# Optimization experiments

Measured on AMD Instinct MI355X. Metric: run time of the kernel, lower is better.

Reference implementation:

```python
import jax, jax.numpy as jnp
import numpy as np

B, T, C = 2, 2048, 1024
E = 1024          # total attention embedding (head_size arg of TransformerBlock)
H = 16            # n_heads
HS = E // H       # per-head size = 64
FF = 4 * C        # ffwd_mul * in_embd
EPS = 1e-5


def setup_inputs() -> dict:
    key = jax.random.key(0)
    ks = jax.random.split(key, 20)
    s = lambda fan_in: 1.0 / np.sqrt(fan_in)
    return {
        "x":     jax.random.normal(ks[0], (B, T, C), jnp.float32),
        "Wq":    jax.random.normal(ks[1], (C, E), jnp.float32) * s(C),
        "bq":    jnp.zeros((E,), jnp.float32),
        "Wk":    jax.random.normal(ks[2], (C, E), jnp.float32) * s(C),
        "bk":    jnp.zeros((E,), jnp.float32),
        "Wv":    jax.random.normal(ks[3], (C, E), jnp.float32) * s(C),
        "bv":    jnp.zeros((E,), jnp.float32),
        "Wo":    jax.random.normal(ks[4], (E, C), jnp.float32) * s(E),
        "bo":    jnp.zeros((C,), jnp.float32),
        "ln1_g": jnp.ones((C,), jnp.float32),
        "ln1_b": jnp.zeros((C,), jnp.float32),
        "W1":    jax.random.normal(ks[5], (C, FF), jnp.float32) * s(C),
        "b1":    jnp.zeros((FF,), jnp.float32),
        "W2":    jax.random.normal(ks[6], (FF, C), jnp.float32) * s(FF),
        "b2":    jnp.zeros((C,), jnp.float32),
        "ln2_g": jnp.ones((C,), jnp.float32),
        "ln2_b": jnp.zeros((C,), jnp.float32),
        "Wc":    jax.random.normal(ks[7], (C, C), jnp.float32) * s(C),
        "bc":    jnp.zeros((C,), jnp.float32),
    }


def _layernorm(x, g, b):
    mu = jnp.mean(x, axis=-1, keepdims=True)
    var = jnp.mean(jnp.square(x - mu), axis=-1, keepdims=True)
    return (x - mu) * jax.lax.rsqrt(var + EPS) * g + b


def _attention(x, Wq, bq, Wk, bk, Wv, bv, Wo, bo):
    # batched equivalent of the per-head Linear q/k/v loop + concat
    q = (x @ Wq + bq).reshape(B, T, H, HS)
    k = (x @ Wk + bk).reshape(B, T, H, HS)
    v = (x @ Wv + bv).reshape(B, T, H, HS)
    scores = jnp.einsum("bthd,bshd->bhts", q, k) / np.sqrt(HS)  # no causal mask in source
    wei = jax.nn.softmax(scores, axis=-1)
    out = jnp.einsum("bhts,bshd->bthd", wei, v).reshape(B, T, E)
    return out @ Wo + bo


def reference(x, Wq, bq, Wk, bk, Wv, bv, Wo, bo, ln1_g, ln1_b,
              W1, b1, W2, b2, ln2_g, ln2_b, Wc, bc):
    out = _layernorm(x + _attention(x, Wq, bq, Wk, bk, Wv, bv, Wo, bo), ln1_g, ln1_b)
    ff = jax.nn.gelu(out @ W1 + b1, approximate=False) @ W2 + b2  # torch GELU is exact erf
    out = _layernorm(out + ff, ln2_g, ln2_b)
    # Conv1d(C, C, kernel_size=1) over transposed input == pointwise linear
    out = out @ Wc.T + bc
    return out
```

## Files before the change

### kernel.cpp

```cpp
#include <hip/hip_runtime.h>
#include <hip/hip_bf16.h>
#include <cstdint>
#include <cstddef>

#define DEVINL __device__ __forceinline__

typedef __attribute__((ext_vector_type(4)))  float f32x4;
typedef __attribute__((ext_vector_type(16))) float f32x16;
typedef __attribute__((ext_vector_type(8)))  short s16x8;

#define QSCALE 0.1803368801111204f

DEVINL short f2bf(float f) {
  union { float f; unsigned u; } v; v.f = f;
  unsigned r = (v.u + 0x7fffu + ((v.u >> 16) & 1u)) >> 16;
  return (short)r;
}

DEVINL void gload_lds16(const void* g, void* l) {
  __builtin_amdgcn_global_load_lds((const __attribute__((address_space(1))) void*)g,
                                   (__attribute__((address_space(3))) void*)l,
                                   16, 0, 0);
}

DEVINL s16x8 lds_frag(const short* base, int row, int cb) {
  const int addr = row * 128 + (cb ^ ((row & 7) << 4));
  return *(const s16x8*)((const char*)base + addr);
}

enum { EPI_F32 = 0, EPI_GELU = 1, EPI_RES = 2, EPI_QKV = 3 };

template <int EPI, int BM>
__global__ __launch_bounds__(256) void gemm_bt(
    const short* __restrict__ A, const short* __restrict__ Bt,
    const float* __restrict__ bias, const float* __restrict__ res,
    float* __restrict__ outF, short* __restrict__ outB,
    short* __restrict__ qp, short* __restrict__ kp, short* __restrict__ vt,
    int M, int N, int K)
{
  constexpr int MI = BM / 32;
  constexpr int CAW = BM / 64;
  __shared__ short As[BM * 32];
  __shared__ short Bs[128 * 32];
  const int tid = threadIdx.x;
  const int w = tid >> 6, lane = tid & 63;
  const int wr = w >> 1, wc = w & 1;

  const int gx = gridDim.x;
  int id = blockIdx.x + gx * blockIdx.y;
  const int cpx = (gx * gridDim.y) >> 3;
  id = (id & 7) * cpx + (id >> 3);
  const int n0 = (id % gx) * 128, m0 = (id / gx) * BM;

  const int lrow = lane >> 2, lk = (lane & 3) << 3;
  const short* Ag = A + (size_t)m0 * K;
  const short* Bg = Bt + (size_t)n0 * K;

  f32x4 acc[MI][4] = {};

  for (int kk = 0; kk < K; kk += 32) {
#pragma unroll
    for (int i = 0; i < CAW; ++i) {
      const int c = w * CAW + i;
      gload_lds16(Ag + (size_t)(c * 16 + lrow) * K + (kk + lk), &As[c * 512]);
    }
#pragma unroll
    for (int i = 0; i < 2; ++i) {
      const int c = w * 2 + i;
      gload_lds16(Bg + (size_t)(c * 16 + lrow) * K + (kk + lk), &Bs[c * 512]);
    }
    __syncthreads();
    s16x8 af[MI], bf[4];
#pragma unroll
    for (int mi = 0; mi < MI; ++mi)
      af[mi] = *(const s16x8*)&As[(wr * (BM / 2) + mi * 16 + (lane & 15)) * 32 + ((lane >> 4) << 3)];
#pragma unroll
    for (int ni = 0; ni < 4; ++ni)
      bf[ni] = *(const s16x8*)&Bs[(wc * 64 + ni * 16 + (lane & 15)) * 32 + ((lane >> 4) << 3)];
#pragma unroll
    for (int mi = 0; mi < MI; ++mi)
#pragma unroll
      for (int ni = 0; ni < 4; ++ni)
        acc[mi][ni] = __builtin_amdgcn_mfma_f32_16x16x32_bf16(af[mi], bf[ni], acc[mi][ni], 0, 0, 0);
    __syncthreads();
  }

  const int rbase = m0 + wr * (BM / 2) + ((lane >> 4) << 2);
  const int cbase = n0 + wc * 64 + (lane & 15);
#pragma unroll
  for (int mi = 0; mi < MI; ++mi) {
#pragma unroll
    for (int ni = 0; ni < 4; ++ni) {
      const int col = cbase + ni * 16;
      const float bv = bias[col];
      if (EPI == EPI_QKV) {
        const int e = col & 1023, id3 = col >> 10;
        const int h = e >> 6, d = e & 63;
        const int row0 = rbase + mi * 16;
        const int b = row0 >> 11, t0 = row0 & 2047;
        if (id3 == 0) {
#pragma unroll
          for (int j = 0; j < 4; ++j)
            qp[((size_t)(b * 16 + h) * 2048 + t0 + j) * 64 + d] = f2bf((acc[mi][ni][j] + bv) * QSCALE);
        } else if (id3 == 1) {
#pragma unroll
          for (int j = 0; j < 4; ++j)
            kp[((size_t)(b * 16 + h) * 2048 + t0 + j) * 64 + d] = f2bf(acc[mi][ni][j] + bv);
        } else {
          short4 pk4;
          pk4.x = f2bf(acc[mi][ni][0] + bv); pk4.y = f2bf(acc[mi][ni][1] + bv);
          pk4.z = f2bf(acc[mi][ni][2] + bv); pk4.w = f2bf(acc[mi][ni][3] + bv);
          *(short4*)&vt[((size_t)(b * 16 + h) * 64 + d) * 2048 + t0] = pk4;
        }
      } else {
#pragma unroll
        for (int j = 0; j < 4; ++j) {
          const int row = rbase + mi * 16 + j;
          float v = acc[mi][ni][j] + bv;
          if (EPI == EPI_GELU) {
            outB[(size_t)row * N + col] = f2bf(0.5f * v * (1.0f + erff(v * 0.70710678118654752f)));
          } else if (EPI == EPI_RES) {
            outF[(size_t)row * N + col] = v + res[(size_t)row * N + col];
          } else {
            outF[(size_t)row * N + col] = v;
          }
        }
      }
    }
  }
}

__global__ __launch_bounds__(256) void attn_kernel(
    const short* __restrict__ qg, const short* __restrict__ kg,
    const short* __restrict__ vtg, short* __restrict__ outB)
{
  __shared__ short Ks[2][64 * 64];
  __shared__ short Vs[2][64 * 64];
  __shared__ float sbuf[4][32];

  const int bh = blockIdx.x, qb = blockIdx.y;
  const int tid = threadIdx.x, w = tid >> 6, lane = tid & 63;
  const int b = bh >> 4, h = bh & 15;
  const int ql = lane & 31, hi = lane >> 5;
  const int qrow = qb * 128 + w * 32 + ql;

  s16x8 qf[4];
  const short* qrp = qg + ((size_t)bh * 2048 + qrow) * 64;
#pragma unroll
  for (int kd = 0; kd < 4; ++kd)
    qf[kd] = *(const s16x8*)(qrp + kd * 16 + hi * 8);

  f32x16 o[2] = {};
  float mrow = -3.0e38f, lsum = 0.f;

  const size_t kbase = (size_t)bh * 2048 * 64;
  const size_t vbase = (size_t)bh * 64 * 2048;

#define STAGE(t, bufi)                                                         \
  {                                                                            \
    _Pragma("unroll") for (int i = 0; i < 2; ++i) {                            \
      const int pb = i * 4096 + w * 1024;                                      \
      const int p = pb + lane * 16;                                            \
      const int row = p >> 7;                                                  \
      const int cs = (p & 127) ^ ((row & 7) << 4);                             \
      gload_lds16(kg + kbase + (size_t)((t) * 64 + row) * 64 + (cs >> 1),      \
                  &Ks[bufi][pb >> 1]);                                         \
      gload_lds16(vtg + vbase + (size_t)row * 2048 + (t) * 64 + (cs >> 1),     \
                  &Vs[bufi][pb >> 1]);                                         \
    }                                                                          \
  }

  STAGE(0, 0);
  __syncthreads();

  for (int t = 0; t < 32; ++t) {
    const int buf = t & 1;
    if (t < 31) STAGE(t + 1, buf ^ 1);
    const short* kb = Ks[buf];
    const short* vb = Vs[buf];

    f32x16 pS[2] = {};
#pragma unroll
    for (int kd = 0; kd < 4; ++kd) {
      const s16x8 a0 = lds_frag(kb, ql,      kd * 32 + hi * 16);
      const s16x8 a1 = lds_frag(kb, 32 + ql, kd * 32 + hi * 16);
      pS[0] = __builtin_amdgcn_mfma_f32_32x32x16_bf16(a0, qf[kd], pS[0], 0, 0, 0);
      pS[1] = __builtin_amdgcn_mfma_f32_32x32x16_bf16(a1, qf[kd], pS[1], 0, 0, 0);
    }

    float pm = pS[0][0];
#pragma unroll
    for (int r = 1; r < 16; ++r) pm = fmaxf(pm, pS[0][r]);
#pragma unroll
    for (int r = 0; r < 16; ++r) pm = fmaxf(pm, pS[1][r]);
    pm = fmaxf(pm, __shfl_xor(pm, 32));

    if (!__all(pm <= mrow + 8.0f)) {
      const float mnew = fmaxf(mrow, pm);
      const float alpha = exp2f(mrow - mnew);
      mrow = mnew;
      lsum *= alpha;
      sbuf[w][ql] = alpha;
#pragma unroll
      for (int r = 0; r < 16; ++r) {
        const float a = sbuf[w][(r & 3) + 8 * (r >> 2) + 4 * hi];
        o[0][r] *= a; o[1][r] *= a;
      }
    }

    float rs = 0.f;
#pragma unroll
    for (int r = 0; r < 16; ++r) { pS[0][r] = exp2f(pS[0][r] - mrow); rs += pS[0][r]; }
#pragma unroll
    for (int r = 0; r < 16; ++r) { pS[1][r] = exp2f(pS[1][r] - mrow); rs += pS[1][r]; }
    rs += __shfl_xor(rs, 32);
    lsum += rs;

#pragma unroll
    for (int ks = 0; ks < 4; ++ks) {
      const int tI = ks >> 1, b8 = (ks & 1) * 8;
      unsigned u0, u1, v0, v1;
      asm("v_cvt_pk_bf16_f32 %0, %1, %2" : "=v"(u0) : "v"(pS[tI][b8 + 0]), "v"(pS[tI][b8 + 1]));
      asm("v_cvt_pk_bf16_f32 %0, %1, %2" : "=v"(u1) : "v"(pS[tI][b8 + 2]), "v"(pS[tI][b8 + 3]));
      asm("v_cvt_pk_bf16_f32 %0, %1, %2" : "=v"(v0) : "v"(pS[tI][b8 + 4]), "v"(pS[tI][b8 + 5]));
      asm("v_cvt_pk_bf16_f32 %0, %1, %2" : "=v"(v1) : "v"(pS[tI][b8 + 6]), "v"(pS[tI][b8 + 7]));
      const unsigned su0 = (unsigned)__shfl_xor((int)u0, 32);
      const unsigned su1 = (unsigned)__shfl_xor((int)u1, 32);
      const unsigned sv0 = (unsigned)__shfl_xor((int)v0, 32);
      const unsigned sv1 = (unsigned)__shfl_xor((int)v1, 32);
      union { unsigned u[4]; s16x8 s; } pa;
      pa.u[0] = hi ? sv0 : u0;
      pa.u[1] = hi ? sv1 : u1;
      pa.u[2] = hi ? v0 : su0;
      pa.u[3] = hi ? v1 : su1;
      const s16x8 vf0 = lds_frag(vb, ql,      ks * 32 + hi * 16);
      const s16x8 vf1 = lds_frag(vb, 32 + ql, ks * 32 + hi * 16);
      o[0] = __builtin_amdgcn_mfma_f32_32x32x16_bf16(pa.s, vf0, o[0], 0, 0, 0);
      o[1] = __builtin_amdgcn_mfma_f32_32x32x16_bf16(pa.s, vf1, o[1], 0, 0, 0);
    }
    __syncthreads();
  }

  sbuf[w][ql] = lsum;
#pragma unroll
  for (int r = 0; r < 16; ++r) {
    const int q = (r & 3) + 8 * (r >> 2) + 4 * hi;
    const float linv = 1.0f / sbuf[w][q];
    const int tq = qb * 128 + w * 32 + q;
    const size_t orow = ((size_t)b * 2048 + tq) * 1024 + h * 64;
    outB[orow + ql]      = f2bf(o[0][r] * linv);
    outB[orow + 32 + ql] = f2bf(o[1][r] * linv);
  }
}

__global__ __launch_bounds__(256) void ln_kernel(
    const float* in, float* outF, short* __restrict__ outB,
    const float* __restrict__ gw, const float* __restrict__ bw)
{
  const int row = blockIdx.x, tid = threadIdx.x;
  const float4 v = ((const float4*)(in + (size_t)row * 1024))[tid];
  float s = v.x + v.y + v.z + v.w;
  float s2 = v.x * v.x + v.y * v.y + v.z * v.z + v.w * v.w;
#pragma unroll
  for (int m = 1; m < 64; m <<= 1) { s += __shfl_xor(s, m); s2 += __shfl_xor(s2, m); }
  __shared__ float as1[4], as2[4];
  if ((tid & 63) == 0) { as1[tid >> 6] = s; as2[tid >> 6] = s2; }
  __syncthreads();
  s = as1[0] + as1[1] + as1[2] + as1[3];
  s2 = as2[0] + as2[1] + as2[2] + as2[3];
  const float mu = s * (1.f / 1024.f);
  const float var = s2 * (1.f / 1024.f) - mu * mu;
  const float rstd = rsqrtf(var + 1e-5f);
  const float4 g = ((const float4*)gw)[tid];
  const float4 bb = ((const float4*)bw)[tid];
  float4 y;
  y.x = (v.x - mu) * rstd * g.x + bb.x;
  y.y = (v.y - mu) * rstd * g.y + bb.y;
  y.z = (v.z - mu) * rstd * g.z + bb.z;
  y.w = (v.w - mu) * rstd * g.w + bb.w;
  ((float4*)(outF + (size_t)row * 1024))[tid] = y;
  short4 ob; ob.x = f2bf(y.x); ob.y = f2bf(y.y); ob.z = f2bf(y.z); ob.w = f2bf(y.w);
  ((short4*)(outB + (size_t)row * 1024))[tid] = ob;
}

__global__ __launch_bounds__(256) void transpose_cast(
    const float* __restrict__ src, short* __restrict__ dst, int R, int Cc)
{
  __shared__ float tile[32][33];
  const int c0 = blockIdx.x * 32, r0 = blockIdx.y * 32;
  const int x = threadIdx.x & 31, y = threadIdx.x >> 5;
#pragma unroll
  for (int i = 0; i < 32; i += 8)
    tile[y + i][x] = src[(size_t)(r0 + y + i) * Cc + c0 + x];
  __syncthreads();
#pragma unroll
  for (int i = 0; i < 32; i += 8)
    dst[(size_t)(c0 + y + i) * R + r0 + x] = f2bf(tile[x][y + i]);
}

__global__ __launch_bounds__(256) void cast_bf16_kernel(
    const float* __restrict__ src, short* __restrict__ dst, int n4)
{
  const int i = blockIdx.x * 256 + threadIdx.x;
  if (i < n4) {
    const float4 v = ((const float4*)src)[i];
    short4 o; o.x = f2bf(v.x); o.y = f2bf(v.y); o.z = f2bf(v.z); o.w = f2bf(v.w);
    ((short4*)dst)[i] = o;
  }
}

__global__ void concat3_kernel(const float* a, const float* b, const float* c, float* o)
{
  const int i = blockIdx.x * 256 + threadIdx.x;
  if (i < 3072) o[i] = (i < 1024 ? a[i] : (i < 2048 ? b[i - 1024] : c[i - 2048]));
}

extern "C" void kernel_launch(void* const* d_in, const int* in_sizes, int n_in,
                              void* d_out, int out_size, void* d_ws, size_t ws_size,
                              hipStream_t stream)
{
  const float* x    = (const float*)d_in[0];
  const float* Wq   = (const float*)d_in[1];
  const float* bq   = (const float*)d_in[2];
  const float* Wk   = (const float*)d_in[3];
  const float* bk   = (const float*)d_in[4];
  const float* Wv   = (const float*)d_in[5];
  const float* bv   = (const float*)d_in[6];
  const float* Wo   = (const float*)d_in[7];
  const float* bo   = (const float*)d_in[8];
  const float* ln1g = (const float*)d_in[9];
  const float* ln1b = (const float*)d_in[10];
  const float* W1   = (const float*)d_in[11];
  const float* b1   = (const float*)d_in[12];
  const float* W2   = (const float*)d_in[13];
  const float* b2   = (const float*)d_in[14];
  const float* ln2g = (const float*)d_in[15];
  const float* ln2b = (const float*)d_in[16];
  const float* Wc   = (const float*)d_in[17];
  const float* bc   = (const float*)d_in[18];
  float* out = (float*)d_out;

  char* p = (char*)d_ws;
  auto alloc = [&](size_t bytes) { char* r = p; p += (bytes + 255) & ~(size_t)255; return r; };

  short* qkvT = (short*)alloc((size_t)3072 * 1024 * 2);
  short* WoT  = (short*)alloc((size_t)1024 * 1024 * 2);
  short* W1T  = (short*)alloc((size_t)4096 * 1024 * 2);
  short* W2T  = (short*)alloc((size_t)1024 * 4096 * 2);
  short* WcB  = (short*)alloc((size_t)1024 * 1024 * 2);
  float* bqkv = (float*)alloc(3072 * 4);
  short* xb   = (short*)alloc((size_t)4096 * 1024 * 2);
  short* qb_  = (short*)alloc((size_t)32 * 2048 * 64 * 2);
  short* kb_  = (short*)alloc((size_t)32 * 2048 * 64 * 2);
  short* vt_  = (short*)alloc((size_t)32 * 64 * 2048 * 2);
  short* ff1  = xb;
  short* attnO= (short*)alloc((size_t)4096 * 1024 * 2);
  float* h1   = (float*)alloc((size_t)4096 * 1024 * 4);
  short* o1b  = (short*)alloc((size_t)4096 * 1024 * 2);
  float* h2   = (float*)alloc((size_t)4096 * 1024 * 4);
  short* o2b  = (short*)alloc((size_t)4096 * 1024 * 2);

  cast_bf16_kernel<<<4096, 256, 0, stream>>>(x, xb, 1048576);
  transpose_cast<<<dim3(32, 32),  256, 0, stream>>>(Wq, qkvT,                1024, 1024);
  transpose_cast<<<dim3(32, 32),  256, 0, stream>>>(Wk, qkvT + 1024 * 1024,  1024, 1024);
  transpose_cast<<<dim3(32, 32),  256, 0, stream>>>(Wv, qkvT + 2048 * 1024,  1024, 1024);
  transpose_cast<<<dim3(32, 32),  256, 0, stream>>>(Wo, WoT,                 1024, 1024);
  transpose_cast<<<dim3(128, 32), 256, 0, stream>>>(W1, W1T,                 1024, 4096);
  transpose_cast<<<dim3(32, 128), 256, 0, stream>>>(W2, W2T,                 4096, 1024);
  cast_bf16_kernel<<<1024, 256, 0, stream>>>(Wc, WcB, 262144);
  concat3_kernel<<<12, 256, 0, stream>>>(bq, bk, bv, bqkv);

  gemm_bt<EPI_QKV, 128><<<dim3(24, 32), 256, 0, stream>>>(
      xb, qkvT, bqkv, nullptr, nullptr, nullptr, qb_, kb_, vt_, 4096, 3072, 1024);
  attn_kernel<<<dim3(32, 16), 256, 0, stream>>>(qb_, kb_, vt_, attnO);
  gemm_bt<EPI_RES, 64><<<dim3(8, 64), 256, 0, stream>>>(
      attnO, WoT, bo, x, h1, nullptr, nullptr, nullptr, nullptr, 4096, 1024, 1024);
  ln_kernel<<<4096, 256, 0, stream>>>(h1, h1, o1b, ln1g, ln1b);
  gemm_bt<EPI_GELU, 128><<<dim3(32, 32), 256, 0, stream>>>(
      o1b, W1T, b1, nullptr, nullptr, ff1, nullptr, nullptr, nullptr, 4096, 4096, 1024);
  gemm_bt<EPI_RES, 64><<<dim3(8, 64), 256, 0, stream>>>(
      ff1, W2T, b2, h1, h2, nullptr, nullptr, nullptr, nullptr, 4096, 1024, 4096);
  ln_kernel<<<4096, 256, 0, stream>>>(h2, h2, o2b, ln2g, ln2b);
  gemm_bt<EPI_F32, 64><<<dim3(8, 64), 256, 0, stream>>>(
      o2b, WcB, bc, nullptr, out, nullptr, nullptr, nullptr, nullptr, 4096, 1024, 1024);
}
```

Before: 467.7 us.

## Double-buffer GEMM LDS tiles and raise wave priority around MFMA blocks

The GEMM kernel now keeps two LDS buffers for its A and B tiles and issues the global-to-LDS loads for the next K step before computing on the current one. This removes the load-then-wait stall each iteration and leaves a single barrier per step. Both the GEMM and attention kernels also wrap their MFMA sequences in s_setprio(1)/s_setprio(0) to favour waves that are issuing matrix work. The extra buffers double the GEMM's LDS use, which may lower occupancy.

```diff
diff --git a/kernel.cpp b/kernel.cpp
--- a/kernel.cpp
+++ b/kernel.cpp
@@ -40,8 +40,8 @@
 {
   constexpr int MI = BM / 32;
   constexpr int CAW = BM / 64;
-  __shared__ short As[BM * 32];
-  __shared__ short Bs[128 * 32];
+  __shared__ short As[2][BM * 32];
+  __shared__ short Bs[2][128 * 32];
   const int tid = threadIdx.x;
   const int w = tid >> 6, lane = tid & 63;
   const int wr = w >> 1, wc = w & 1;
@@ -56,34 +56,46 @@
   const short* Ag = A + (size_t)m0 * K;
   const short* Bg = Bt + (size_t)n0 * K;
 
+#define GSTAGE(kk, bufi)                                                     \
+  {                                                                          \
+    _Pragma("unroll") for (int i = 0; i < CAW; ++i) {                        \
+      const int c = w * CAW + i;                                             \
+      gload_lds16(Ag + (size_t)(c * 16 + lrow) * K + ((kk) + lk),            \
+                  &As[bufi][c * 512]);                                       \
+    }                                                                        \
+    _Pragma("unroll") for (int i = 0; i < 2; ++i) {                          \
+      const int c = w * 2 + i;                                               \
+      gload_lds16(Bg + (size_t)(c * 16 + lrow) * K + ((kk) + lk),            \
+                  &Bs[bufi][c * 512]);                                       \
+    }                                                                        \
+  }
+
   f32x4 acc[MI][4] = {};
 
+  GSTAGE(0, 0);
+  __syncthreads();
+  int cur = 0;
+
   for (int kk = 0; kk < K; kk += 32) {
-#pragma unroll
-    for (int i = 0; i < CAW; ++i) {
-      const int c = w * CAW + i;
-      gload_lds16(Ag + (size_t)(c * 16 + lrow) * K + (kk + lk), &As[c * 512]);
-    }
-#pragma unroll
-    for (int i = 0; i < 2; ++i) {
-      const int c = w * 2 + i;
-      gload_lds16(Bg + (size_t)(c * 16 + lrow) * K + (kk + lk), &Bs[c * 512]);
-    }
-    __syncthreads();
+    if (kk + 32 < K) GSTAGE(kk + 32, cur ^ 1);
     s16x8 af[MI], bf[4];
 #pragma unroll
     for (int mi = 0; mi < MI; ++mi)
-      af[mi] = *(const s16x8*)&As[(wr * (BM / 2) + mi * 16 + (lane & 15)) * 32 + ((lane >> 4) << 3)];
+      af[mi] = *(const s16x8*)&As[cur][(wr * (BM / 2) + mi * 16 + (lane & 15)) * 32 + ((lane >> 4) << 3)];
 #pragma unroll
     for (int ni = 0; ni < 4; ++ni)
-      bf[ni] = *(const s16x8*)&Bs[(wc * 64 + ni * 16 + (lane & 15)) * 32 + ((lane >> 4) << 3)];
+      bf[ni] = *(const s16x8*)&Bs[cur][(wc * 64 + ni * 16 + (lane & 15)) * 32 + ((lane >> 4) << 3)];
+    __builtin_amdgcn_s_setprio(1);
 #pragma unroll
     for (int mi = 0; mi < MI; ++mi)
 #pragma unroll
       for (int ni = 0; ni < 4; ++ni)
         acc[mi][ni] = __builtin_amdgcn_mfma_f32_16x16x32_bf16(af[mi], bf[ni], acc[mi][ni], 0, 0, 0);
+    __builtin_amdgcn_s_setprio(0);
     __syncthreads();
-  }
+    cur ^= 1;
+  }
+#undef GSTAGE
 
   const int rbase = m0 + wr * (BM / 2) + ((lane >> 4) << 2);
   const int cbase = n0 + wc * 64 + (lane & 15);
@@ -180,6 +192,7 @@
     const short* vb = Vs[buf];
 
     f32x16 pS[2] = {};
+    __builtin_amdgcn_s_setprio(1);
 #pragma unroll
     for (int kd = 0; kd < 4; ++kd) {
       const s16x8 a0 = lds_frag(kb, ql,      kd * 32 + hi * 16);
@@ -187,6 +200,7 @@
       pS[0] = __builtin_amdgcn_mfma_f32_32x32x16_bf16(a0, qf[kd], pS[0], 0, 0, 0);
       pS[1] = __builtin_amdgcn_mfma_f32_32x32x16_bf16(a1, qf[kd], pS[1], 0, 0, 0);
     }
+    __builtin_amdgcn_s_setprio(0);
 
     float pm = pS[0][0];
 #pragma unroll
@@ -235,8 +249,10 @@
       pa.u[3] = hi ? v1 : su1;
       const s16x8 vf0 = lds_frag(vb, ql,      ks * 32 + hi * 16);
       const s16x8 vf1 = lds_frag(vb, 32 + ql, ks * 32 + hi * 16);
+      __builtin_amdgcn_s_setprio(1);
       o[0] = __builtin_amdgcn_mfma_f32_32x32x16_bf16(pa.s, vf0, o[0], 0, 0, 0);
       o[1] = __builtin_amdgcn_mfma_f32_32x32x16_bf16(pa.s, vf1, o[1], 0, 0, 0);
+      __builtin_amdgcn_s_setprio(0);
     }
     __syncthreads();
   }
```

Measured after the change: 454.6 us. -2.8%, faster.
